# Kernel optimization log

Hardware: AMD Instinct MI355X
Metric: run time of the kernel (lower is better)

Reference implementation:

```python
import jax, jax.numpy as jnp
import numpy as np

K = 6            # kmer length
NF = 8192        # n_filters (> 4**K so kmer_params has shape (NF, 4, K))
M = 4 ** K       # 4096 kmers
B = 1024         # batch


def setup_inputs() -> dict:
    key = jax.random.key(0)
    k1, k2 = jax.random.split(key)
    freq = jax.random.uniform(k1, (B, M), dtype=jnp.float32)          # kmer frequencies (B, 4^k)
    kmer_params = jax.random.normal(k2, (NF, 4, K), dtype=jnp.float32)
    temperature = jnp.ones((1,), dtype=jnp.float32)
    # base-4 digits of arange(4^k), most-significant first == itertools.product order
    pos = 4 ** jnp.arange(K - 1, -1, -1)
    kmer_idcs = ((jnp.arange(M)[:, None] // pos[None, :]) % 4).astype(jnp.int32)  # (M, K)
    return {"freq": freq, "kmer_params": kmer_params,
            "temperature": temperature, "kmer_idcs": kmer_idcs}


def reference(freq, kmer_params, temperature, kmer_idcs):
    k = kmer_params.shape[-1]
    # matches[f, i] = sum_j kmer_params[f, kmer_idcs[i, j], j]
    # Advanced indexing broadcasts (M, k) indices against arange(k): result (F, M, k).
    # This replaces torch's expand-to-(F, M, 1, k) + gather + squeeze + sum(-1).
    matches = kmer_params[:, kmer_idcs, jnp.arange(k)].sum(axis=-1)   # (F, M)
    probs = jax.nn.softmax(matches / temperature, axis=1)             # softmax over kmers
    pooled = freq @ probs.T                                           # (B, F)
    profile = pooled / pooled.sum(axis=1, keepdims=True)
    return profile
```

## Files before the change

kernel.cpp:

```cpp
#include <hip/hip_runtime.h>


typedef __bf16  bf16x8 __attribute__((ext_vector_type(8)));
typedef float   f32x4  __attribute__((ext_vector_type(4)));

#define GLD16(gp, lp)                                                          \
  __builtin_amdgcn_global_load_lds(                                            \
      (const __attribute__((address_space(1))) void*)(gp),                     \
      (__attribute__((address_space(3))) void*)(lp), 16, 0, 0)

__device__ __forceinline__ short f2bf(float x) {
  unsigned u = __float_as_uint(x);
  unsigned r = (u + 0x7fffu + ((u >> 16) & 1u)) >> 16;
  return (short)r;
}

__device__ __forceinline__ float wave_max(float v) {
  #pragma unroll
  for (int off = 32; off; off >>= 1) v = fmaxf(v, __shfl_xor(v, off, 64));
  return v;
}
__device__ __forceinline__ float wave_sum(float v) {
  #pragma unroll
  for (int off = 32; off; off >>= 1) v += __shfl_xor(v, off, 64);
  return v;
}

__global__ __launch_bounds__(256) void cast_kernel(const float* __restrict__ in,
                                                   short* __restrict__ out) {
  int idx = blockIdx.x * 256 + threadIdx.x;
  float4 v = ((const float4*)in)[idx];
  short4 o;
  o.x = f2bf(v.x); o.y = f2bf(v.y); o.z = f2bf(v.z); o.w = f2bf(v.w);
  ((short4*)out)[idx] = o;
}

__global__ __launch_bounds__(256) void tables_kernel(const float* __restrict__ kp,
                                                     const float* __restrict__ temp,
                                                     float* __restrict__ E1t,
                                                     float* __restrict__ E2) {
  const int t = threadIdx.x;
  const int lane = t & 63, wave = t >> 6;
  const int f = blockIdx.x * 4 + wave;
  const float* P = kp + f * 24;
  const int d0 = (lane >> 4) & 3, d1 = (lane >> 2) & 3, d2 = lane & 3;
  const float thi = P[d0 * 6 + 0] + P[d1 * 6 + 1] + P[d2 * 6 + 2];
  const float tlo = P[d0 * 6 + 3] + P[d1 * 6 + 4] + P[d2 * 6 + 5];
  const float mxhi = wave_max(thi), mxlo = wave_max(tlo);
  const float invT = 1.0f / temp[0];
  const float e1 = __expf((thi - mxhi) * invT);
  const float e2 = __expf((tlo - mxlo) * invT);
  const float s1 = wave_sum(e1), s2 = wave_sum(e2);
  const float invZ = 1.0f / (s1 * s2);
  E1t[lane * 8192 + f] = e1 * invZ;
  E2[(size_t)f * 64 + lane] = e2;
}

__global__ __launch_bounds__(512, 2) void gemm_kernel(const short* __restrict__ A,
                                                      const float* __restrict__ E1t,
                                                      const float* __restrict__ E2,
                                                      float* __restrict__ C) {
  __shared__ short As[3 * 128 * 64];

  const int t = threadIdx.x;
  const int lane = t & 63, wave = t >> 6;
  const int quad = lane >> 4, l16 = lane & 15;
  const int m0 = blockIdx.y * 128;
  const int n0 = blockIdx.x * 256;
  const int wm = (wave >> 2) * 64;
  const int wn = (wave & 3) * 64;

  f32x4 acc[4][4];
  #pragma unroll
  for (int i = 0; i < 4; i++)
    #pragma unroll
    for (int j = 0; j < 4; j++) acc[i][j] = (f32x4){0.f, 0.f, 0.f, 0.f};

  int nrow[4];
  #pragma unroll
  for (int j = 0; j < 4; j++) nrow[j] = n0 + wn + j * 16 + l16;
  float4 e2a[4][2], e2b[4][2];
  #pragma unroll
  for (int j = 0; j < 4; j++)
    #pragma unroll
    for (int ks = 0; ks < 2; ks++) {
      const float* p = E2 + (size_t)nrow[j] * 64 + (ks * 4 + quad) * 8;
      e2a[j][ks] = *(const float4*)p;
      e2b[j][ks] = *(const float4*)(p + 4);
    }

  const int lane_row = lane >> 3;
  const int src_col = ((lane & 7) ^ lane_row) * 8;
  const int sw = l16 & 7;

  const int r0 = wave * 16;
  const short* Abase = A + (size_t)(m0 + r0 + lane_row) * 4096 + src_col;

  #define STAGE(kt, buf) do {                                                  \
    const short* g_ = Abase + (kt) * 64;                                       \
    GLD16(g_,            &As[(buf) * 8192 + r0 * 64 + lane * 8]);              \
    GLD16(g_ + 8 * 4096, &As[(buf) * 8192 + (r0 + 8) * 64 + lane * 8]);        \
  } while (0)

  float e1n[4], e1c[4];
  STAGE(0, 0);
  #pragma unroll
  for (int j = 0; j < 4; j++) e1n[j] = E1t[nrow[j]];
  STAGE(1, 1);

  int cb = 0, sb = 2;

  #pragma unroll 1
  for (int kt = 0; kt < 64; ++kt) {
    asm volatile("s_waitcnt vmcnt(2)" ::: "memory");
    __builtin_amdgcn_s_barrier();
    asm volatile("" ::: "memory");

    #pragma unroll
    for (int j = 0; j < 4; j++) e1c[j] = e1n[j];
    const int tn = (kt + 1 > 63) ? 63 : kt + 1;
    #pragma unroll
    for (int j = 0; j < 4; j++) e1n[j] = E1t[tn * 8192 + nrow[j]];
    const int ts = (kt + 2 > 63) ? 63 : kt + 2;
    STAGE(ts, sb);

    const short* buf = &As[cb * 8192];

    bf16x8 a[4][2];
    #pragma unroll
    for (int i = 0; i < 4; i++)
      #pragma unroll
      for (int ks = 0; ks < 2; ks++)
        a[i][ks] = *(const bf16x8*)&buf[(wm + i * 16 + l16) * 64 +
                                        (((ks * 4 + quad) ^ sw) * 8)];

    #pragma unroll
    for (int j = 0; j < 4; j++) {
      bf16x8 b[2];
      #pragma unroll
      for (int ks = 0; ks < 2; ks++) {
        const float s = e1c[j];
        bf16x8 bb;
        bb[0] = (__bf16)(s * e2a[j][ks].x);
        bb[1] = (__bf16)(s * e2a[j][ks].y);
        bb[2] = (__bf16)(s * e2a[j][ks].z);
        bb[3] = (__bf16)(s * e2a[j][ks].w);
        bb[4] = (__bf16)(s * e2b[j][ks].x);
        bb[5] = (__bf16)(s * e2b[j][ks].y);
        bb[6] = (__bf16)(s * e2b[j][ks].z);
        bb[7] = (__bf16)(s * e2b[j][ks].w);
        b[ks] = bb;
      }
      __builtin_amdgcn_s_setprio(1);
      #pragma unroll
      for (int ks = 0; ks < 2; ks++)
        #pragma unroll
        for (int i = 0; i < 4; i++)
          acc[i][j] = __builtin_amdgcn_mfma_f32_16x16x32_bf16(a[i][ks], b[ks],
                                                              acc[i][j], 0, 0, 0);
      __builtin_amdgcn_s_setprio(0);
    }

    cb = (cb + 1 == 3) ? 0 : cb + 1;
    sb = (sb + 1 == 3) ? 0 : sb + 1;
  }

  asm volatile("s_waitcnt vmcnt(0)" ::: "memory");

  #pragma unroll
  for (int i = 0; i < 4; i++) {
    #pragma unroll
    for (int r = 0; r < 4; r++) {
      const int brow = m0 + wm + i * 16 + quad * 4 + r;
      float* crow = C + (size_t)brow * 8192 + n0 + wn + l16;
      #pragma unroll
      for (int j = 0; j < 4; j++) crow[j * 16] = acc[i][j][r];
    }
  }
  #undef STAGE
}

__global__ __launch_bounds__(256) void norm_kernel(float* __restrict__ out) {
  const int b = blockIdx.x;
  const int t = threadIdx.x;
  const int lane = t & 63, wave = t >> 6;
  __shared__ float red[4];

  float4* row = (float4*)(out + (size_t)b * 8192);
  float4 v[8];
  float s = 0.0f;
  #pragma unroll
  for (int q = 0; q < 8; q++) {
    v[q] = row[q * 256 + t];
    s += (v[q].x + v[q].y) + (v[q].z + v[q].w);
  }
  float ws = wave_sum(s);
  if (lane == 0) red[wave] = ws;
  __syncthreads();
  float tot = (red[0] + red[1]) + (red[2] + red[3]);
  float inv = 1.0f / tot;
  #pragma unroll
  for (int q = 0; q < 8; q++) {
    v[q].x *= inv; v[q].y *= inv; v[q].z *= inv; v[q].w *= inv;
    row[q * 256 + t] = v[q];
  }
}

extern "C" void kernel_launch(void* const* d_in, const int* in_sizes, int n_in,
                              void* d_out, int out_size, void* d_ws, size_t ws_size,
                              hipStream_t stream) {
  const float* freq    = (const float*)d_in[0];
  const float* kparams = (const float*)d_in[1];
  const float* temp    = (const float*)d_in[2];

  float* out = (float*)d_out;

  short* freqb = (short*)d_ws;
  float* E1t   = (float*)(freqb + (size_t)1024 * 4096);
  float* E2    = E1t + (size_t)64 * 8192;

  cast_kernel  <<<4096, 256, 0, stream>>>(freq, freqb);
  tables_kernel<<<2048, 256, 0, stream>>>(kparams, temp, E1t, E2);
  gemm_kernel  <<<dim3(32, 8), 512, 0, stream>>>(freqb, E1t, E2, out);
  norm_kernel  <<<1024, 256, 0, stream>>>(out);
}
```

Baseline: 179.6 us.

## Retile GEMM to 256x128 blocks with split-phase MFMA schedule and LDS-staged E1

The GEMM block tile changes from 128x256 to 256x128, so each block holds more freq rows in LDS and fewer E2-derived columns. The E1 scale table for the block's columns is preloaded into LDS once instead of being fetched from global memory every k-step. Each k-iteration is split into two half-phases, each with its own barriers, so A-tile loads for the next stage interleave with MFMA work in a ping-pong style. This raises LDS use and adds barriers per iteration, which may limit overlap or occupancy.

After: 169.5 us. 5.6% less time.

```diff
diff --git a/kernel.cpp b/kernel.cpp
--- a/kernel.cpp
+++ b/kernel.cpp
@@ -60,15 +60,16 @@
                                                       const float* __restrict__ E1t,
                                                       const float* __restrict__ E2,
                                                       float* __restrict__ C) {
-  __shared__ short As[3 * 128 * 64];
+  __shared__ short As[3 * 256 * 64];
+  __shared__ float E1s[64 * 128];
 
   const int t = threadIdx.x;
   const int lane = t & 63, wave = t >> 6;
   const int quad = lane >> 4, l16 = lane & 15;
-  const int m0 = blockIdx.y * 128;
-  const int n0 = blockIdx.x * 256;
-  const int wm = (wave >> 2) * 64;
-  const int wn = (wave & 3) * 64;
+  const int m0 = blockIdx.y * 256;
+  const int n0 = blockIdx.x * 128;
+  const int wm = (wave & 3) * 64;
+  const int wn = (wave >> 2) * 64;
 
   f32x4 acc[4][4];
   #pragma unroll
@@ -93,50 +94,47 @@
   const int src_col = ((lane & 7) ^ lane_row) * 8;
   const int sw = l16 & 7;
 
-  const int r0 = wave * 16;
-  const short* Abase = A + (size_t)(m0 + r0 + lane_row) * 4096 + src_col;
-
-  #define STAGE(kt, buf) do {                                                  \
-    const short* g_ = Abase + (kt) * 64;                                       \
-    GLD16(g_,            &As[(buf) * 8192 + r0 * 64 + lane * 8]);              \
-    GLD16(g_ + 8 * 4096, &As[(buf) * 8192 + (r0 + 8) * 64 + lane * 8]);        \
-  } while (0)
-
-  float e1n[4], e1c[4];
-  STAGE(0, 0);
-  #pragma unroll
-  for (int j = 0; j < 4; j++) e1n[j] = E1t[nrow[j]];
-  STAGE(1, 1);
+  const short* Abase = A + (size_t)(m0 + 32 * wave + lane_row) * 4096 + src_col;
+  #define STG(kt, buf, c)                                                      \
+    GLD16(Abase + (size_t)(8 * (c)) * 4096 + (kt) * 64,                        \
+          &As[(buf) * 16384 + (32 * wave + 8 * (c)) * 64 + lane * 8])
+
+  {
+    const int r2 = 2 * wave;
+    const float* esrc = E1t + (size_t)r2 * 8192 + n0 + (lane & 31) * 4
+                        + (size_t)(lane >> 5) * 8192;
+    #pragma unroll
+    for (int q = 0; q < 4; q++)
+      GLD16(esrc + (size_t)q * 16 * 8192, &E1s[(q * 16 + r2) * 128]);
+  }
+  #pragma unroll
+  for (int c = 0; c < 4; c++) STG(0, 0, c);
+  #pragma unroll
+  for (int c = 0; c < 4; c++) STG(1, 1, c);
+  asm volatile("s_waitcnt vmcnt(4)" ::: "memory");
+  __builtin_amdgcn_s_barrier();
 
   int cb = 0, sb = 2;
 
   #pragma unroll 1
   for (int kt = 0; kt < 64; ++kt) {
-    asm volatile("s_waitcnt vmcnt(2)" ::: "memory");
-    __builtin_amdgcn_s_barrier();
-    asm volatile("" ::: "memory");
-
-    #pragma unroll
-    for (int j = 0; j < 4; j++) e1c[j] = e1n[j];
-    const int tn = (kt + 1 > 63) ? 63 : kt + 1;
-    #pragma unroll
-    for (int j = 0; j < 4; j++) e1n[j] = E1t[tn * 8192 + nrow[j]];
+    const short* buf = &As[cb * 16384];
     const int ts = (kt + 2 > 63) ? 63 : kt + 2;
-    STAGE(ts, sb);
-
-    const short* buf = &As[cb * 8192];
-
-    bf16x8 a[4][2];
-    #pragma unroll
-    for (int i = 0; i < 4; i++)
+
+    bf16x8 a0[2][2];
+    #pragma unroll
+    for (int i = 0; i < 2; i++)
       #pragma unroll
       for (int ks = 0; ks < 2; ks++)
-        a[i][ks] = *(const bf16x8*)&buf[(wm + i * 16 + l16) * 64 +
-                                        (((ks * 4 + quad) ^ sw) * 8)];
-
-    #pragma unroll
-    for (int j = 0; j < 4; j++) {
-      bf16x8 b[2];
+        a0[i][ks] = *(const bf16x8*)&buf[(wm + i * 16 + l16) * 64 +
+                                         (((ks * 4 + quad) ^ sw) * 8)];
+    float e1c[4];
+    #pragma unroll
+    for (int j = 0; j < 4; j++) e1c[j] = E1s[kt * 128 + wn + j * 16 + l16];
+
+    bf16x8 b[2][4];
+    #pragma unroll
+    for (int j = 0; j < 4; j++)
       #pragma unroll
       for (int ks = 0; ks < 2; ks++) {
         const float s = e1c[j];
@@ -149,17 +147,50 @@
         bb[5] = (__bf16)(s * e2b[j][ks].y);
         bb[6] = (__bf16)(s * e2b[j][ks].z);
         bb[7] = (__bf16)(s * e2b[j][ks].w);
-        b[ks] = bb;
+        b[ks][j] = bb;
       }
-      __builtin_amdgcn_s_setprio(1);
+
+    STG(ts, sb, 0);
+    STG(ts, sb, 1);
+
+    __builtin_amdgcn_s_barrier();
+    __builtin_amdgcn_sched_barrier(0);
+    __builtin_amdgcn_s_setprio(1);
+    #pragma unroll
+    for (int j = 0; j < 4; j++)
+      #pragma unroll
+      for (int i = 0; i < 2; i++)
+        #pragma unroll
+        for (int ks = 0; ks < 2; ks++)
+          acc[i][j] = __builtin_amdgcn_mfma_f32_16x16x32_bf16(a0[i][ks], b[ks][j],
+                                                              acc[i][j], 0, 0, 0);
+    __builtin_amdgcn_s_setprio(0);
+    __builtin_amdgcn_s_barrier();
+
+    bf16x8 a1[2][2];
+    #pragma unroll
+    for (int i = 0; i < 2; i++)
       #pragma unroll
       for (int ks = 0; ks < 2; ks++)
+        a1[i][ks] = *(const bf16x8*)&buf[(wm + 32 + i * 16 + l16) * 64 +
+                                         (((ks * 4 + quad) ^ sw) * 8)];
+    STG(ts, sb, 2);
+    STG(ts, sb, 3);
+
+    asm volatile("s_waitcnt vmcnt(4)" ::: "memory");
+    __builtin_amdgcn_s_barrier();
+    __builtin_amdgcn_sched_barrier(0);
+    __builtin_amdgcn_s_setprio(1);
+    #pragma unroll
+    for (int j = 0; j < 4; j++)
+      #pragma unroll
+      for (int i = 0; i < 2; i++)
         #pragma unroll
-        for (int i = 0; i < 4; i++)
-          acc[i][j] = __builtin_amdgcn_mfma_f32_16x16x32_bf16(a[i][ks], b[ks],
-                                                              acc[i][j], 0, 0, 0);
-      __builtin_amdgcn_s_setprio(0);
-    }
+        for (int ks = 0; ks < 2; ks++)
+          acc[i + 2][j] = __builtin_amdgcn_mfma_f32_16x16x32_bf16(a1[i][ks], b[ks][j],
+                                                                  acc[i + 2][j], 0, 0, 0);
+    __builtin_amdgcn_s_setprio(0);
+    __builtin_amdgcn_s_barrier();
 
     cb = (cb + 1 == 3) ? 0 : cb + 1;
     sb = (sb + 1 == 3) ? 0 : sb + 1;
@@ -177,7 +208,7 @@
       for (int j = 0; j < 4; j++) crow[j * 16] = acc[i][j][r];
     }
   }
-  #undef STAGE
+  #undef STG
 }
 
 __global__ __launch_bounds__(256) void norm_kernel(float* __restrict__ out) {
@@ -221,6 +252,6 @@
 
   cast_kernel  <<<4096, 256, 0, stream>>>(freq, freqb);
   tables_kernel<<<2048, 256, 0, stream>>>(kparams, temp, E1t, E2);
-  gemm_kernel  <<<dim3(32, 8), 512, 0, stream>>>(freqb, E1t, E2, out);
+  gemm_kernel  <<<dim3(64, 4), 512, 0, stream>>>(freqb, E1t, E2, out);
   norm_kernel  <<<1024, 256, 0, stream>>>(out);
 }
```

## Hoist E2 bf16 fragments and apply E1 scale after per-chunk MFMA

Applied to the files above, without the earlier changes.

The GEMM now converts the E2 factor to bf16 fragments once, outside the k-loop, and runs two MFMAs per k-tile into a zero accumulator. It then scales that partial product by the E1 value in fp32 before adding it to the accumulator. This removes the per-iteration multiply-and-convert that built B fragments, at the cost of extra vector FMAs on the accumulators. The tile shrinks to 64x256 with 4 waves, staging is now double-buffered with a second barrier per iteration, and the grid doubles to 512 blocks.

Result: faster. 159.3 us (-11.3%).

```diff
diff --git a/kernel.cpp b/kernel.cpp
--- a/kernel.cpp
+++ b/kernel.cpp
@@ -56,19 +56,18 @@
   E2[(size_t)f * 64 + lane] = e2;
 }
 
-__global__ __launch_bounds__(512, 2) void gemm_kernel(const short* __restrict__ A,
+__global__ __launch_bounds__(256, 2) void gemm_kernel(const short* __restrict__ A,
                                                       const float* __restrict__ E1t,
                                                       const float* __restrict__ E2,
                                                       float* __restrict__ C) {
-  __shared__ short As[3 * 128 * 64];
+  __shared__ short As[2][64 * 64];
 
   const int t = threadIdx.x;
   const int lane = t & 63, wave = t >> 6;
   const int quad = lane >> 4, l16 = lane & 15;
-  const int m0 = blockIdx.y * 128;
+  const int m0 = blockIdx.y * 64;
   const int n0 = blockIdx.x * 256;
-  const int wm = (wave >> 2) * 64;
-  const int wn = (wave & 3) * 64;
+  const int wn = wave * 64;
 
   f32x4 acc[4][4];
   #pragma unroll
@@ -79,90 +78,76 @@
   int nrow[4];
   #pragma unroll
   for (int j = 0; j < 4; j++) nrow[j] = n0 + wn + j * 16 + l16;
-  float4 e2a[4][2], e2b[4][2];
+  bf16x8 e2f[2][4];
   #pragma unroll
   for (int j = 0; j < 4; j++)
     #pragma unroll
     for (int ks = 0; ks < 2; ks++) {
       const float* p = E2 + (size_t)nrow[j] * 64 + (ks * 4 + quad) * 8;
-      e2a[j][ks] = *(const float4*)p;
-      e2b[j][ks] = *(const float4*)(p + 4);
+      float4 lo = *(const float4*)p, hi = *(const float4*)(p + 4);
+      bf16x8 bb;
+      bb[0] = (__bf16)lo.x; bb[1] = (__bf16)lo.y;
+      bb[2] = (__bf16)lo.z; bb[3] = (__bf16)lo.w;
+      bb[4] = (__bf16)hi.x; bb[5] = (__bf16)hi.y;
+      bb[6] = (__bf16)hi.z; bb[7] = (__bf16)hi.w;
+      e2f[ks][j] = bb;
     }
 
   const int lane_row = lane >> 3;
   const int src_col = ((lane & 7) ^ lane_row) * 8;
   const int sw = l16 & 7;
-
-  const int r0 = wave * 16;
-  const short* Abase = A + (size_t)(m0 + r0 + lane_row) * 4096 + src_col;
-
-  #define STAGE(kt, buf) do {                                                  \
-    const short* g_ = Abase + (kt) * 64;                                       \
-    GLD16(g_,            &As[(buf) * 8192 + r0 * 64 + lane * 8]);              \
-    GLD16(g_ + 8 * 4096, &As[(buf) * 8192 + (r0 + 8) * 64 + lane * 8]);        \
+  const int chunk = wave * 2;
+  const short* Abase = A + (size_t)(m0 + lane_row) * 4096 + src_col;
+
+  #define STG(kt, buf) do {                                                    \
+    GLD16(Abase + (size_t)((chunk + 0) * 8) * 4096 + (kt) * 64,                \
+          &As[buf][(chunk + 0) * 512 + lane * 8]);                             \
+    GLD16(Abase + (size_t)((chunk + 1) * 8) * 4096 + (kt) * 64,                \
+          &As[buf][(chunk + 1) * 512 + lane * 8]);                             \
   } while (0)
 
+  STG(0, 0);
   float e1n[4], e1c[4];
-  STAGE(0, 0);
   #pragma unroll
   for (int j = 0; j < 4; j++) e1n[j] = E1t[nrow[j]];
-  STAGE(1, 1);
-
-  int cb = 0, sb = 2;
+
+  const f32x4 Z4 = (f32x4){0.f, 0.f, 0.f, 0.f};
 
   #pragma unroll 1
   for (int kt = 0; kt < 64; ++kt) {
-    asm volatile("s_waitcnt vmcnt(2)" ::: "memory");
+    const int cb = kt & 1;
+    const int tn = (kt + 1 > 63) ? 63 : kt + 1;
+
+    STG(tn, cb ^ 1);
+    #pragma unroll
+    for (int j = 0; j < 4; j++) e1c[j] = e1n[j];
+    #pragma unroll
+    for (int j = 0; j < 4; j++) e1n[j] = E1t[tn * 8192 + nrow[j]];
+
+    asm volatile("s_waitcnt vmcnt(6)" ::: "memory");
     __builtin_amdgcn_s_barrier();
-    asm volatile("" ::: "memory");
-
-    #pragma unroll
-    for (int j = 0; j < 4; j++) e1c[j] = e1n[j];
-    const int tn = (kt + 1 > 63) ? 63 : kt + 1;
-    #pragma unroll
-    for (int j = 0; j < 4; j++) e1n[j] = E1t[tn * 8192 + nrow[j]];
-    const int ts = (kt + 2 > 63) ? 63 : kt + 2;
-    STAGE(ts, sb);
-
-    const short* buf = &As[cb * 8192];
 
     bf16x8 a[4][2];
     #pragma unroll
     for (int i = 0; i < 4; i++)
       #pragma unroll
       for (int ks = 0; ks < 2; ks++)
-        a[i][ks] = *(const bf16x8*)&buf[(wm + i * 16 + l16) * 64 +
-                                        (((ks * 4 + quad) ^ sw) * 8)];
-
+        a[i][ks] = *(const bf16x8*)&As[cb][(i * 16 + l16) * 64 +
+                                          (((ks * 4 + quad) ^ sw) * 8)];
+
+    __builtin_amdgcn_s_setprio(1);
     #pragma unroll
     for (int j = 0; j < 4; j++) {
-      bf16x8 b[2];
+      const f32x4 s4 = (f32x4){e1c[j], e1c[j], e1c[j], e1c[j]};
       #pragma unroll
-      for (int ks = 0; ks < 2; ks++) {
-        const float s = e1c[j];
-        bf16x8 bb;
-        bb[0] = (__bf16)(s * e2a[j][ks].x);
-        bb[1] = (__bf16)(s * e2a[j][ks].y);
-        bb[2] = (__bf16)(s * e2a[j][ks].z);
-        bb[3] = (__bf16)(s * e2a[j][ks].w);
-        bb[4] = (__bf16)(s * e2b[j][ks].x);
-        bb[5] = (__bf16)(s * e2b[j][ks].y);
-        bb[6] = (__bf16)(s * e2b[j][ks].z);
-        bb[7] = (__bf16)(s * e2b[j][ks].w);
-        b[ks] = bb;
+      for (int i = 0; i < 4; i++) {
+        f32x4 P = __builtin_amdgcn_mfma_f32_16x16x32_bf16(a[i][0], e2f[0][j], Z4, 0, 0, 0);
+        P = __builtin_amdgcn_mfma_f32_16x16x32_bf16(a[i][1], e2f[1][j], P, 0, 0, 0);
+        acc[i][j] += s4 * P;
       }
-      __builtin_amdgcn_s_setprio(1);
-      #pragma unroll
-      for (int ks = 0; ks < 2; ks++)
-        #pragma unroll
-        for (int i = 0; i < 4; i++)
-          acc[i][j] = __builtin_amdgcn_mfma_f32_16x16x32_bf16(a[i][ks], b[ks],
-                                                              acc[i][j], 0, 0, 0);
-      __builtin_amdgcn_s_setprio(0);
     }
-
-    cb = (cb + 1 == 3) ? 0 : cb + 1;
-    sb = (sb + 1 == 3) ? 0 : sb + 1;
+    __builtin_amdgcn_s_setprio(0);
+    __builtin_amdgcn_s_barrier();
   }
 
   asm volatile("s_waitcnt vmcnt(0)" ::: "memory");
@@ -171,13 +156,13 @@
   for (int i = 0; i < 4; i++) {
     #pragma unroll
     for (int r = 0; r < 4; r++) {
-      const int brow = m0 + wm + i * 16 + quad * 4 + r;
+      const int brow = m0 + i * 16 + quad * 4 + r;
       float* crow = C + (size_t)brow * 8192 + n0 + wn + l16;
       #pragma unroll
       for (int j = 0; j < 4; j++) crow[j * 16] = acc[i][j][r];
     }
   }
-  #undef STAGE
+  #undef STG
 }
 
 __global__ __launch_bounds__(256) void norm_kernel(float* __restrict__ out) {
@@ -221,6 +206,6 @@
 
   cast_kernel  <<<4096, 256, 0, stream>>>(freq, freqb);
   tables_kernel<<<2048, 256, 0, stream>>>(kparams, temp, E1t, E2);
-  gemm_kernel  <<<dim3(32, 8), 512, 0, stream>>>(freqb, E1t, E2, out);
+  gemm_kernel  <<<dim3(32, 16), 256, 0, stream>>>(freqb, E1t, E2, out);
   norm_kernel  <<<1024, 256, 0, stream>>>(out);
 }
```
